# Performance work log

Measured on AMD Instinct MI355X. Metric: run time of the kernel, lower is better.

The kernel has to match this reference:

```python
import jax, jax.numpy as jnp
import numpy as np

GAMMA = -0.1   # l0_gamma
ZETA = 1.1     # l0_zeta
BETA = 0.66    # l0_beta (hard-concrete temperature)
LAMBDA = 0.01  # lambda_reg (post-warmup current_lambda)
EPS = 1e-12


def _layernorm(x, g, b, eps=1e-5):
    mu = jnp.mean(x, axis=-1, keepdims=True)
    var = jnp.var(x, axis=-1, keepdims=True)
    return (x - mu) / jnp.sqrt(var + eps) * g + b


def setup_inputs() -> dict:
    key = jax.random.key(0)
    ks = jax.random.split(key, 12)
    B, N, D, H, E, C = 8, 512, 512, 256, 32, 2
    node_feat = jax.random.normal(ks[0], (B, N, D), jnp.float32)
    labels = jax.random.randint(ks[1], (B,), 0, C)
    a = (jax.random.uniform(ks[2], (B, N, N)) < 0.05).astype(jnp.float32)
    adjs = jnp.maximum(a, jnp.swapaxes(a, 1, 2)) * (1.0 - jnp.eye(N, dtype=jnp.float32))
    masks = jnp.ones((B, N), jnp.float32)
    init = lambda k, shp, fan: jax.random.normal(k, shp, jnp.float32) / np.sqrt(fan).astype(np.float32)
    return {
        "node_feat": node_feat, "labels": labels, "adjs": adjs, "masks": masks,
        # edge scorer MLP: concat([h_i,h_j]) -> edge_dim -> 1, factorized as Wa@h_i + Wb@h_j
        "Wa": init(ks[3], (D, E), D), "Wb": init(ks[4], (D, E), D), "be": jnp.zeros((E,), jnp.float32),
        "W2e": init(ks[5], (E, 1), E), "b2e": jnp.zeros((1,), jnp.float32),
        # conv: Linear(feature_dim, hidden_dim)
        "Wconv": init(ks[6], (D, H), D), "bconv": jnp.zeros((H,), jnp.float32),
        # classifier: Linear(H,H//2) -> ReLU -> LayerNorm -> spectral_norm(Linear(H//2,C))
        "W1c": init(ks[7], (H, H // 2), H), "b1c": jnp.zeros((H // 2,), jnp.float32),
        "ln_g": jnp.ones((H // 2,), jnp.float32), "ln_b": jnp.zeros((H // 2,), jnp.float32),
        "W2c": init(ks[8], (H // 2, C), H // 2), "b2c": jnp.zeros((C,), jnp.float32),
        "u_sn": jax.random.normal(ks[9], (C,), jnp.float32),  # spectral-norm power-iteration buffer
    }


def reference(node_feat, labels, adjs, masks, Wa, Wb, be, W2e, b2e,
              Wconv, bconv, W1c, b1c, ln_g, ln_b, W2c, b2c, u_sn):
    B = node_feat.shape[0]
    # F.normalize(node_feat, p=2, dim=2)
    nrm = jnp.sqrt(jnp.sum(node_feat * node_feat, axis=2, keepdims=True))
    nf = node_feat / jnp.maximum(nrm, EPS)
    # edge scoring: logAlpha[b,i,j] = MLP([h_i ; h_j])
    e1 = nf @ Wa                                  # [B,N,E]
    e2 = nf @ Wb                                  # [B,N,E]
    hpair = jax.nn.relu(e1[:, :, None, :] + e2[:, None, :, :] + be)   # [B,N,N,E]
    logAlpha = jnp.einsum('bije,e->bij', hpair, W2e[:, 0]) + b2e[0]    # [B,N,N]
    # deterministic hard-concrete gate (eval mode): clip(sigmoid(logAlpha)*(zeta-gamma)+gamma, 0, 1)
    gate = jnp.clip(jax.nn.sigmoid(logAlpha) * (ZETA - GAMMA) + GAMMA, 0.0, 1.0)
    edge_weights = gate * adjs
    # aggregate: row-normalized weighted adjacency
    wadj = adjs * edge_weights
    row_sum = jnp.sum(wadj, axis=2, keepdims=True) + 1e-8
    h = jnp.einsum('bij,bjd->bid', wadj / row_sum, nf)
    h = jax.nn.relu(h @ Wconv + bconv)            # [B,N,H]
    # edge-weighted attention pooling: node importance = weighted degree, masked softmax
    imp = jnp.sum(wadj, axis=2)                    # [B,N]
    attn_logits = jnp.where(masks > 0, imp, -1e9)
    attn = jax.nn.softmax(attn_logits, axis=1)
    graph_rep = jnp.einsum('bn,bnh->bh', attn, h)  # [B,H]
    # classifier
    z = jax.nn.relu(graph_rep @ W1c + b1c)
    z = _layernorm(z, ln_g, ln_b)
    # spectral norm (1 power iteration, u/v stop-gradded like torch buffers)
    v = W2c @ u_sn
    v = jax.lax.stop_gradient(v / jnp.maximum(jnp.linalg.norm(v), EPS))
    u2 = W2c.T @ v
    u2 = jax.lax.stop_gradient(u2 / jnp.maximum(jnp.linalg.norm(u2), EPS))
    sigma = v @ (W2c @ u2)
    logits = z @ (W2c / sigma) + b2c              # [B,C]
    # losses
    logp = jax.nn.log_softmax(logits, axis=1)
    cls_loss = -jnp.mean(logp[jnp.arange(B), labels])
    l0_penalty = jnp.sum(jax.nn.sigmoid(logAlpha - BETA * jnp.log(-GAMMA / ZETA)))
    total_loss = cls_loss + LAMBDA * l0_penalty
    return logits, total_loss, adjs * edge_weights
```

## Files before the change

kernel.cpp:

```cpp
#include <hip/hip_runtime.h>


#define Bsz 8
#define Nn  512
#define Dd  512
#define Hh  256
#define Ee  32

#define WS_NFCPK  0L
#define WS_E1     524288L
#define WS_E2     655360L
#define WS_WADJB  786432L
#define WS_RS     1835008L
#define WS_L0     1839104L
#define WS_GR     1839112L
#define WS_WABPK  1841160L
#define WS_WCPK   1857544L

typedef __bf16 bf16x8 __attribute__((ext_vector_type(8)));
typedef float  f32x4  __attribute__((ext_vector_type(4)));

__device__ inline ushort f2bf(float f) {
  union { float f; unsigned u; } c; c.f = f;
  return (ushort)((c.u + 0x7fffu + ((c.u >> 16) & 1u)) >> 16);
}

__global__ __launch_bounds__(256) void pack_weights(
    const float* __restrict__ Wconv, const float* __restrict__ Wa,
    const float* __restrict__ Wb, ushort* __restrict__ wcpk,
    ushort* __restrict__ wabpk)
{
  const int g = blockIdx.x*256 + threadIdx.x;
  if (g < 16384) {
    const int kq = g >> 8, n = g & 255;
    ushort tmp[8];
    #pragma unroll
    for (int j = 0; j < 8; ++j) tmp[j] = f2bf(Wconv[(kq*8 + j)*Hh + n]);
    *(uint4*)(wcpk + (long)g*8) = *(uint4*)tmp;
  } else if (g < 16384 + 4096) {
    const int gg = g - 16384;
    const int kq = gg >> 6, n = gg & 63;
    const float* W = (n < 32) ? Wa : Wb;
    const int e = n & 31;
    ushort tmp[8];
    #pragma unroll
    for (int j = 0; j < 8; ++j) tmp[j] = f2bf(W[(kq*8 + j)*Ee + e]);
    *(uint4*)(wabpk + (long)gg*8) = *(uint4*)tmp;
  }
}

__global__ __launch_bounds__(256) void norm_e12_nfc(
    const float* __restrict__ nfeat, const ushort* __restrict__ wabpk,
    const ushort* __restrict__ wcpk, const float* __restrict__ be,
    ushort* __restrict__ nfcpk, float* __restrict__ e1, float* __restrict__ e2,
    float* __restrict__ row_sum, float* __restrict__ gr,
    float* __restrict__ l0_sum)
{
  const int blk = blockIdx.x;
  const int r0 = blk*16;
  const int b = r0 >> 9;
  const int t = threadIdx.x;
  const int r = t >> 4;
  const int seg = t & 15;

  __shared__ ushort As[(63*17 + 15 + 1)*8];
  __shared__ ushort BsA[2][4*64*8];
  __shared__ ushort BsC[2][4*256*8];

  float4 v[8];
  const float* src = nfeat + (long)(r0 + r)*Dd + seg*32;
  #pragma unroll
  for (int i = 0; i < 8; ++i) v[i] = *(const float4*)(src + i*4);
  float s = 0.f;
  #pragma unroll
  for (int i = 0; i < 8; ++i)
    s += v[i].x*v[i].x + v[i].y*v[i].y + v[i].z*v[i].z + v[i].w*v[i].w;
  #pragma unroll
  for (int m = 1; m < 16; m <<= 1) s += __shfl_xor(s, m, 16);
  const float sc = 1.f / fmaxf(sqrtf(s), 1e-12f);
  #pragma unroll
  for (int q = 0; q < 4; ++q) {
    ushort tmp[8];
    const float4 a = v[2*q], bq = v[2*q+1];
    tmp[0]=f2bf(a.x*sc);  tmp[1]=f2bf(a.y*sc);  tmp[2]=f2bf(a.z*sc);  tmp[3]=f2bf(a.w*sc);
    tmp[4]=f2bf(bq.x*sc); tmp[5]=f2bf(bq.y*sc); tmp[6]=f2bf(bq.z*sc); tmp[7]=f2bf(bq.w*sc);
    *(uint4*)(As + ((seg*4 + q)*17 + r)*8) = *(uint4*)tmp;
  }
  if (t < 16) row_sum[r0 + t] = 0.f;
  if (blk == 0) {
    for (int p = t; p < Bsz*Hh; p += 256) gr[p] = 0.f;
    if (t == 0) *l0_sum = 0.f;
  }

  const int lane = t & 63, l15 = lane & 15, quad = lane >> 4;
  const int w = t >> 6;
  const int abq = t >> 6, abn = t & 63;

  f32x4 acc_e = {0.f, 0.f, 0.f, 0.f};
  f32x4 acc_c[4];
  #pragma unroll
  for (int j = 0; j < 4; ++j) acc_c[j] = (f32x4){0.f,0.f,0.f,0.f};

  uint4 pab = *(const uint4*)(wabpk + ((long)abq*64 + abn)*8);
  uint4 pc[4];
  #pragma unroll
  for (int p = 0; p < 4; ++p) {
    const int g = t + p*256;
    pc[p] = *(const uint4*)(wcpk + ((long)(g >> 8)*256 + (g & 255))*8);
  }
  *(uint4*)(BsA[0] + (abq*64 + abn)*8) = pab;
  #pragma unroll
  for (int p = 0; p < 4; ++p) {
    const int g = t + p*256;
    *(uint4*)(BsC[0] + ((g >> 8)*256 + (g & 255))*8) = pc[p];
  }
  {
    pab = *(const uint4*)(wabpk + ((long)(4 + abq)*64 + abn)*8);
    #pragma unroll
    for (int p = 0; p < 4; ++p) {
      const int g = t + p*256;
      pc[p] = *(const uint4*)(wcpk + ((long)(4 + (g >> 8))*256 + (g & 255))*8);
    }
  }

  for (int k0 = 0; k0 < 512; k0 += 32) {
    const int pb = (k0 >> 5) & 1;
    __syncthreads();
    if (k0 + 32 < 512) {
      *(uint4*)(BsA[1-pb] + (abq*64 + abn)*8) = pab;
      #pragma unroll
      for (int p = 0; p < 4; ++p) {
        const int g = t + p*256;
        *(uint4*)(BsC[1-pb] + ((g >> 8)*256 + (g & 255))*8) = pc[p];
      }
      if (k0 + 64 < 512) {
        const int kb = (k0 + 64) >> 3;
        pab = *(const uint4*)(wabpk + ((long)(kb + abq)*64 + abn)*8);
        #pragma unroll
        for (int p = 0; p < 4; ++p) {
          const int g = t + p*256;
          pc[p] = *(const uint4*)(wcpk + ((long)(kb + (g >> 8))*256 + (g & 255))*8);
        }
      }
    }
    const bf16x8 af = *(const bf16x8*)(As + (((k0 >> 3) + quad)*17 + l15)*8);
    const bf16x8 bfa = *(const bf16x8*)(BsA[pb] + (quad*64 + w*16 + l15)*8);
    acc_e = __builtin_amdgcn_mfma_f32_16x16x32_bf16(af, bfa, acc_e, 0, 0, 0);
    #pragma unroll
    for (int fn = 0; fn < 4; ++fn) {
      const bf16x8 bfc = *(const bf16x8*)(BsC[pb] + (quad*256 + w*64 + fn*16 + l15)*8);
      acc_c[fn] = __builtin_amdgcn_mfma_f32_16x16x32_bf16(af, bfc, acc_c[fn], 0, 0, 0);
    }
  }

  {
    const int col = w*16 + l15;
    #pragma unroll
    for (int rr = 0; rr < 4; ++rr) {
      const int row = r0 + quad*4 + rr;
      if (col < 32) e1[(long)row*Ee + col] = acc_e[rr] + be[col];
      else          e2[(long)row*Ee + (col - 32)] = acc_e[rr];
    }
  }

  __syncthreads();
  ushort* tile = BsC[0];
  #pragma unroll
  for (int fn = 0; fn < 4; ++fn) {
    const int col = w*64 + fn*16 + l15;
    #pragma unroll
    for (int rr = 0; rr < 4; ++rr)
      tile[(quad*4 + rr)*260 + col] = f2bf(acc_c[fn][rr]);
  }
  __syncthreads();
  #pragma unroll
  for (int p = 0; p < 2; ++p) {
    const int g = t + p*256;
    const int oct = g >> 8, c = g & 255;
    ushort tmp[8];
    #pragma unroll
    for (int j = 0; j < 8; ++j) tmp[j] = tile[(oct*8 + j)*260 + c];
    const long og = ((r0 & 511) >> 3) + oct;
    *(uint4*)(nfcpk + ((long)b*16384 + og*256 + c)*8) = *(uint4*)tmp;
  }
}

__global__ __launch_bounds__(256) void edge_kernel(
    const float* __restrict__ e1, const float* __restrict__ e2,
    const float* __restrict__ W2e, const float* __restrict__ b2e,
    const float* __restrict__ adjs, float* __restrict__ out_wadj,
    ushort* __restrict__ wadj_b, float* __restrict__ row_sum,
    float* __restrict__ l0_sum)
{
  const int b  = blockIdx.z;
  const int i0 = blockIdx.y * 32;
  const int j0 = blockIdx.x * 128;
  const int t  = threadIdx.x;

  __shared__ float e2s[32*132];

  #pragma unroll
  for (int itr = 0; itr < 4; ++itr) {
    const int idx = t + itr*256;
    const int kq = idx & 7, jg = idx >> 3;
    const float4 v = *(const float4*)(e2 + ((long)(b*Nn + j0 + jg))*Ee + kq*4);
    e2s[(kq*4+0)*132 + jg] = v.x;
    e2s[(kq*4+1)*132 + jg] = v.y;
    e2s[(kq*4+2)*132 + jg] = v.z;
    e2s[(kq*4+3)*132 + jg] = v.w;
  }

  const int pair  = t >> 4;
  const int jslot = t & 15;
  const int ia = i0 + pair*2;
  const int ib = ia + 1;
  const int ja = jslot*4;
  const int jb = ja + 64;

  float e1af[32], e1bf[32], w2f[32];
  #pragma unroll
  for (int q = 0; q < 8; ++q) {
    *(float4*)(&e1af[q*4]) = *(const float4*)(e1 + ((long)(b*Nn + ia))*Ee + q*4);
    *(float4*)(&e1bf[q*4]) = *(const float4*)(e1 + ((long)(b*Nn + ib))*Ee + q*4);
    *(float4*)(&w2f[q*4])  = *(const float4*)(W2e + q*4);
  }
  const float b2 = b2e[0];
  __syncthreads();

  float acc[2][8] = {};
  #pragma unroll
  for (int k = 0; k < 32; ++k) {
    const float4 va = *(const float4*)(e2s + k*132 + ja);
    const float4 vb = *(const float4*)(e2s + k*132 + jb);
    const float w = w2f[k];
    const float ea = e1af[k], eb = e1bf[k];
    acc[0][0] += fmaxf(ea+va.x, 0.f)*w;
    acc[0][1] += fmaxf(ea+va.y, 0.f)*w;
    acc[0][2] += fmaxf(ea+va.z, 0.f)*w;
    acc[0][3] += fmaxf(ea+va.w, 0.f)*w;
    acc[0][4] += fmaxf(ea+vb.x, 0.f)*w;
    acc[0][5] += fmaxf(ea+vb.y, 0.f)*w;
    acc[0][6] += fmaxf(ea+vb.z, 0.f)*w;
    acc[0][7] += fmaxf(ea+vb.w, 0.f)*w;
    acc[1][0] += fmaxf(eb+va.x, 0.f)*w;
    acc[1][1] += fmaxf(eb+va.y, 0.f)*w;
    acc[1][2] += fmaxf(eb+va.z, 0.f)*w;
    acc[1][3] += fmaxf(eb+va.w, 0.f)*w;
    acc[1][4] += fmaxf(eb+vb.x, 0.f)*w;
    acc[1][5] += fmaxf(eb+vb.y, 0.f)*w;
    acc[1][6] += fmaxf(eb+vb.z, 0.f)*w;
    acc[1][7] += fmaxf(eb+vb.w, 0.f)*w;
  }

  float rs[2] = {0.f, 0.f};
  float l0acc = 0.f;
  #pragma unroll
  for (int ii = 0; ii < 2; ++ii) {
    const int i = (ii == 0) ? ia : ib;
    const float* arow = adjs     + ((long)(b*Nn + i))*Nn + j0;
    ushort* bwrow     = wadj_b   + ((long)(b*Nn + i))*Nn + j0;
    float* outrow     = out_wadj + ((long)(b*Nn + i))*Nn + j0;
    #pragma unroll
    for (int h2 = 0; h2 < 2; ++h2) {
      const int jl = (h2 == 0) ? ja : jb;
      const float4 av = *(const float4*)(arow + jl);
      float wv[4];
      #pragma unroll
      for (int c = 0; c < 4; ++c) {
        const float logA = acc[ii][h2*4 + c] + b2;
        const float sg = 1.f/(1.f + expf(-logA));
        const float gate = fminf(fmaxf(sg*1.2f - 0.1f, 0.f), 1.f);
        const float a = (c==0)?av.x:(c==1)?av.y:(c==2)?av.z:av.w;
        const float w = gate*a*a;
        wv[c] = w;
        rs[ii] += w;
        l0acc += 1.f/(1.f + expf(-(logA + 1.58261088f)));
      }
      ushort4 bw;
      bw.x = f2bf(wv[0]); bw.y = f2bf(wv[1]); bw.z = f2bf(wv[2]); bw.w = f2bf(wv[3]);
      *(ushort4*)(bwrow + jl) = bw;
      outrow[jl+0] = wv[0]; outrow[jl+1] = wv[1];
      outrow[jl+2] = wv[2]; outrow[jl+3] = wv[3];
    }
  }

  #pragma unroll
  for (int m = 1; m < 16; m <<= 1) {
    rs[0] += __shfl_xor(rs[0], m, 16);
    rs[1] += __shfl_xor(rs[1], m, 16);
  }
  if (jslot == 0) {
    atomicAdd(&row_sum[b*Nn + ia], rs[0]);
    atomicAdd(&row_sum[b*Nn + ib], rs[1]);
  }
  #pragma unroll
  for (int m = 1; m < 64; m <<= 1) l0acc += __shfl_xor(l0acc, m, 64);
  if ((t & 63) == 0) atomicAdd(l0_sum, l0acc);
}

__global__ __launch_bounds__(256) void gemm_pool(
    const ushort* __restrict__ wadjb, const ushort* __restrict__ nfcpk,
    const float* __restrict__ row_sum, const float* __restrict__ masks,
    const float* __restrict__ bconv, float* __restrict__ gr)
{
  const int bb = blockIdx.z;
  const int m0 = blockIdx.y*64, n0 = blockIdx.x*64;
  const int t = threadIdx.x;
  const int lane = t & 63, l15 = lane & 15, quad = lane >> 4;
  const int wv = t >> 6, wr = wv & 1, wc = wv >> 1;

  __shared__ ushort As[2][259*8];
  __shared__ ushort Bs[2][256*8];
  __shared__ float ptile[64*65];
  __shared__ float red[256];
  __shared__ float attn_s[64];
  __shared__ float mx_s, sinv_s;

  const ushort* Ab = wadjb + (long)bb*262144;
  const ushort* Bb = nfcpk + (long)bb*131072;
  const int am = t >> 2, akq = t & 3;
  const int bn = t & 63, bkq = t >> 6;

  f32x4 acc[2][2];
  #pragma unroll
  for (int i = 0; i < 2; ++i)
    #pragma unroll
    for (int j = 0; j < 2; ++j) acc[i][j] = (f32x4){0.f,0.f,0.f,0.f};

  uint4 ra = *(const uint4*)(Ab + (long)(m0+am)*512 + akq*8);
  uint4 rb = *(const uint4*)(Bb + ((long)bkq*256 + n0 + bn)*8);
  *(uint4*)(As[0] + (akq*65 + am)*8) = ra;
  *(uint4*)(Bs[0] + (bkq*64 + bn)*8) = rb;
  ra = *(const uint4*)(Ab + (long)(m0+am)*512 + 32 + akq*8);
  rb = *(const uint4*)(Bb + ((long)(4 + bkq)*256 + n0 + bn)*8);

  for (int k0 = 0; k0 < 512; k0 += 32) {
    const int pb = (k0 >> 5) & 1;
    __syncthreads();
    if (k0 + 32 < 512) {
      *(uint4*)(As[1-pb] + (akq*65 + am)*8) = ra;
      *(uint4*)(Bs[1-pb] + (bkq*64 + bn)*8) = rb;
      if (k0 + 64 < 512) {
        ra = *(const uint4*)(Ab + (long)(m0+am)*512 + (k0+64) + akq*8);
        rb = *(const uint4*)(Bb + ((long)(((k0+64) >> 3) + bkq)*256 + n0 + bn)*8);
      }
    }
    bf16x8 af[2], bfr[2];
    #pragma unroll
    for (int i = 0; i < 2; ++i)
      af[i] = *(const bf16x8*)(As[pb] + (quad*65 + wr*32 + i*16 + l15)*8);
    #pragma unroll
    for (int j = 0; j < 2; ++j)
      bfr[j] = *(const bf16x8*)(Bs[pb] + (quad*64 + wc*32 + j*16 + l15)*8);
    #pragma unroll
    for (int i = 0; i < 2; ++i)
      #pragma unroll
      for (int j = 0; j < 2; ++j)
        acc[i][j] = __builtin_amdgcn_mfma_f32_16x16x32_bf16(
            af[i], bfr[j], acc[i][j], 0, 0, 0);
  }
  __syncthreads();

  {
    const float mk0 = masks[bb*Nn + t], mk1 = masks[bb*Nn + t + 256];
    const float lv0 = (mk0 > 0.f) ? row_sum[bb*Nn + t] : -1e9f;
    const float lv1 = (mk1 > 0.f) ? row_sum[bb*Nn + t + 256] : -1e9f;
    red[t] = fmaxf(lv0, lv1); __syncthreads();
    for (int s = 128; s > 0; s >>= 1) { if (t < s) red[t] = fmaxf(red[t], red[t+s]); __syncthreads(); }
    if (t == 0) mx_s = red[0];
    __syncthreads();
    const float mx = mx_s;
    red[t] = expf(lv0 - mx) + expf(lv1 - mx); __syncthreads();
    for (int s = 128; s > 0; s >>= 1) { if (t < s) red[t] += red[t+s]; __syncthreads(); }
    if (t == 0) sinv_s = 1.f/red[0];
    __syncthreads();
    if (t < 64) {
      const int node = m0 + t;
      const float mm = masks[bb*Nn + node];
      const float lv = (mm > 0.f) ? row_sum[bb*Nn + node] : -1e9f;
      attn_s[t] = expf(lv - mx)*sinv_s;
    }
    __syncthreads();
  }

  #pragma unroll
  for (int i = 0; i < 2; ++i) {
    #pragma unroll
    for (int j = 0; j < 2; ++j) {
      const int lcol = wc*32 + j*16 + l15;
      const float bias = bconv[n0 + lcol];
      #pragma unroll
      for (int rr = 0; rr < 4; ++rr) {
        const int lrow = wr*32 + i*16 + quad*4 + rr;
        const int row = m0 + lrow;
        const float scl = 1.f/(row_sum[bb*Nn + row] + 1e-8f);
        const float hv = fmaxf(acc[i][j][rr]*scl + bias, 0.f);
        ptile[lrow*65 + lcol] = hv * attn_s[lrow];
      }
    }
  }
  __syncthreads();
  if (t < 64) {
    float s = 0.f;
    #pragma unroll 4
    for (int rr = 0; rr < 64; ++rr) s += ptile[rr*65 + t];
    atomicAdd(&gr[bb*Hh + n0 + t], s);
  }
}

__global__ __launch_bounds__(256) void classifier_kernel(
    const float* __restrict__ gr, const float* __restrict__ W1c,
    const float* __restrict__ b1c, const float* __restrict__ ln_g,
    const float* __restrict__ ln_b, const float* __restrict__ W2c,
    const float* __restrict__ b2c, const float* __restrict__ u_sn,
    const int* __restrict__ labels, const float* __restrict__ l0_sum,
    float* __restrict__ out)
{
  const int t = threadIdx.x;
  __shared__ float grs[2048];
  __shared__ float z[8][128];
  __shared__ float red[256];
  __shared__ float vv[128];
  __shared__ float mu_s[8], ri_s[8];
  __shared__ float lg[16];
  for (int p = t; p < 2048; p += 256) grs[p] = gr[p];
  __syncthreads();
  #pragma unroll
  for (int p = 0; p < 4; ++p) {
    const int idx = t + p*256;
    const int b = idx >> 7, o = idx & 127;
    float acc = b1c[o];
    for (int d = 0; d < 256; ++d) acc += grs[b*256 + d]*W1c[d*128 + o];
    z[b][o] = fmaxf(acc, 0.f);
  }
  __syncthreads();
  if (t < 8) {
    float mu = 0.f;
    for (int o = 0; o < 128; ++o) mu += z[t][o];
    mu *= (1.f/128.f);
    float var = 0.f;
    for (int o = 0; o < 128; ++o) { const float d = z[t][o]-mu; var += d*d; }
    var *= (1.f/128.f);
    mu_s[t] = mu; ri_s[t] = rsqrtf(var + 1e-5f);
  }
  const float u0 = u_sn[0], u1 = u_sn[1];
  float vt = 0.f;
  if (t < 128) { vt = W2c[2*t]*u0 + W2c[2*t+1]*u1; vv[t] = vt; }
  red[t] = (t < 128) ? vt*vt : 0.f;
  __syncthreads();
  for (int s = 128; s > 0; s >>= 1) { if (t < s) red[t] += red[t+s]; __syncthreads(); }
  const float vninv = 1.f/fmaxf(sqrtf(red[0]), 1e-12f);
  __syncthreads();
  red[t] = (t < 128) ? W2c[2*t]*vv[t]*vninv : 0.f;
  __syncthreads();
  for (int s = 128; s > 0; s >>= 1) { if (t < s) red[t] += red[t+s]; __syncthreads(); }
  const float u20 = red[0];
  __syncthreads();
  red[t] = (t < 128) ? W2c[2*t+1]*vv[t]*vninv : 0.f;
  __syncthreads();
  for (int s = 128; s > 0; s >>= 1) { if (t < s) red[t] += red[t+s]; __syncthreads(); }
  const float u21 = red[0];
  __syncthreads();
  const float uninv = 1.f/fmaxf(sqrtf(u20*u20 + u21*u21), 1e-12f);
  const float u2n0 = u20*uninv, u2n1 = u21*uninv;
  red[t] = (t < 128) ? vv[t]*vninv*(W2c[2*t]*u2n0 + W2c[2*t+1]*u2n1) : 0.f;
  __syncthreads();
  for (int s = 128; s > 0; s >>= 1) { if (t < s) red[t] += red[t+s]; __syncthreads(); }
  const float sinv = 1.f/red[0];
  __syncthreads();
  if (t < 16) {
    const int b = t >> 1, c = t & 1;
    const float mu = mu_s[b], ri = ri_s[b];
    float acc = 0.f;
    for (int o = 0; o < 128; ++o) {
      const float zln = (z[b][o]-mu)*ri*ln_g[o] + ln_b[o];
      acc += zln*W2c[2*o + c];
    }
    const float lgv = acc*sinv + b2c[c];
    lg[t] = lgv;
    out[t] = lgv;
  }
  __syncthreads();
  if (t == 0) {
    float closs = 0.f;
    for (int b = 0; b < 8; ++b) {
      const float a0 = lg[2*b], a1 = lg[2*b+1];
      const float m = fmaxf(a0, a1);
      const float lse = m + logf(expf(a0-m) + expf(a1-m));
      closs += lse - lg[2*b + labels[b]];
    }
    closs *= (1.f/8.f);
    out[16] = closs + 0.01f*l0_sum[0];
  }
}

extern "C" void kernel_launch(void* const* d_in, const int* in_sizes, int n_in,
                              void* d_out, int out_size, void* d_ws, size_t ws_size,
                              hipStream_t stream) {
  const float* node_feat = (const float*)d_in[0];
  const int*   labels    = (const int*)d_in[1];
  const float* adjs      = (const float*)d_in[2];
  const float* masks     = (const float*)d_in[3];
  const float* Wa        = (const float*)d_in[4];
  const float* Wb        = (const float*)d_in[5];
  const float* be        = (const float*)d_in[6];
  const float* W2e       = (const float*)d_in[7];
  const float* b2e       = (const float*)d_in[8];
  const float* Wconv     = (const float*)d_in[9];
  const float* bconv     = (const float*)d_in[10];
  const float* W1c       = (const float*)d_in[11];
  const float* b1c       = (const float*)d_in[12];
  const float* ln_g      = (const float*)d_in[13];
  const float* ln_b      = (const float*)d_in[14];
  const float* W2c       = (const float*)d_in[15];
  const float* b2c       = (const float*)d_in[16];
  const float* u_sn      = (const float*)d_in[17];

  float* out = (float*)d_out;
  float* ws  = (float*)d_ws;
  ushort* nfcpk  = (ushort*)(ws + WS_NFCPK);
  float*  e1     = ws + WS_E1;
  float*  e2     = ws + WS_E2;
  ushort* wadjb  = (ushort*)(ws + WS_WADJB);
  float*  row_sum= ws + WS_RS;
  float*  l0s    = ws + WS_L0;
  float*  gr     = ws + WS_GR;
  ushort* wabpk  = (ushort*)(ws + WS_WABPK);
  ushort* wcpk   = (ushort*)(ws + WS_WCPK);

  pack_weights<<<80, 256, 0, stream>>>(Wconv, Wa, Wb, wcpk, wabpk);
  norm_e12_nfc<<<256, 256, 0, stream>>>(node_feat, wabpk, wcpk, be, nfcpk,
                                        e1, e2, row_sum, gr, l0s);
  edge_kernel<<<dim3(Nn/128, Nn/32, Bsz), 256, 0, stream>>>(
      e1, e2, W2e, b2e, adjs, out + 17, wadjb, row_sum, l0s);
  gemm_pool<<<dim3(Hh/64, Nn/64, Bsz), 256, 0, stream>>>(
      wadjb, nfcpk, row_sum, masks, bconv, gr);
  classifier_kernel<<<1, 256, 0, stream>>>(gr, W1c, b1c, ln_g, ln_b, W2c, b2c,
                                           u_sn, labels, l0s, out);
}
```

Baseline: 195.3 us.

## Replace shared-memory tree reductions with wave shuffles and reuse sigmoid exponential

The edge kernel now reuses the single exp(-logA) for the L0 penalty sigmoid, using exp(-(x+c)) = exp(-x)*exp(-c), which halves transcendental calls per edge. The pooling kernel's softmax max and sum reductions and the classifier kernel's layernorm, spectral-norm and logit reductions switch from barrier-heavy shared-memory trees to wavefront shuffle reductions with a few shared partials. The change targets instruction count and the long chains of __syncthreads in these small kernels. Numerics change slightly because summation order differs and the exp factoring introduces small rounding differences.

Result: slower. 212.7 us (+8.9%).

```diff
diff --git a/kernel.cpp b/kernel.cpp
--- a/kernel.cpp
+++ b/kernel.cpp
@@ -268,13 +268,14 @@
       #pragma unroll
       for (int c = 0; c < 4; ++c) {
         const float logA = acc[ii][h2*4 + c] + b2;
-        const float sg = 1.f/(1.f + expf(-logA));
+        const float e = expf(-logA);
+        const float sg = 1.f/(1.f + e);
         const float gate = fminf(fmaxf(sg*1.2f - 0.1f, 0.f), 1.f);
         const float a = (c==0)?av.x:(c==1)?av.y:(c==2)?av.z:av.w;
         const float w = gate*a*a;
         wv[c] = w;
         rs[ii] += w;
-        l0acc += 1.f/(1.f + expf(-(logA + 1.58261088f)));
+        l0acc += 1.f/(1.f + 0.20543832f*e);
       }
       ushort4 bw;
       bw.x = f2bf(wv[0]); bw.y = f2bf(wv[1]); bw.z = f2bf(wv[2]); bw.w = f2bf(wv[3]);
@@ -312,9 +313,8 @@
   __shared__ ushort As[2][259*8];
   __shared__ ushort Bs[2][256*8];
   __shared__ float ptile[64*65];
-  __shared__ float red[256];
+  __shared__ float red[8];
   __shared__ float attn_s[64];
-  __shared__ float mx_s, sinv_s;
 
   const ushort* Ab = wadjb + (long)bb*262144;
   const ushort* Bb = nfcpk + (long)bb*131072;
@@ -365,20 +365,23 @@
     const float mk0 = masks[bb*Nn + t], mk1 = masks[bb*Nn + t + 256];
     const float lv0 = (mk0 > 0.f) ? row_sum[bb*Nn + t] : -1e9f;
     const float lv1 = (mk1 > 0.f) ? row_sum[bb*Nn + t + 256] : -1e9f;
-    red[t] = fmaxf(lv0, lv1); __syncthreads();
-    for (int s = 128; s > 0; s >>= 1) { if (t < s) red[t] = fmaxf(red[t], red[t+s]); __syncthreads(); }
-    if (t == 0) mx_s = red[0];
+    float m = fmaxf(lv0, lv1);
+    #pragma unroll
+    for (int s = 1; s < 64; s <<= 1) m = fmaxf(m, __shfl_xor(m, s, 64));
+    if (lane == 0) red[wv] = m;
     __syncthreads();
-    const float mx = mx_s;
-    red[t] = expf(lv0 - mx) + expf(lv1 - mx); __syncthreads();
-    for (int s = 128; s > 0; s >>= 1) { if (t < s) red[t] += red[t+s]; __syncthreads(); }
-    if (t == 0) sinv_s = 1.f/red[0];
+    const float mx = fmaxf(fmaxf(red[0], red[1]), fmaxf(red[2], red[3]));
+    float sm = expf(lv0 - mx) + expf(lv1 - mx);
+    #pragma unroll
+    for (int s = 1; s < 64; s <<= 1) sm += __shfl_xor(sm, s, 64);
+    if (lane == 0) red[4 + wv] = sm;
     __syncthreads();
+    const float sinv = 1.f/(red[4] + red[5] + red[6] + red[7]);
     if (t < 64) {
       const int node = m0 + t;
       const float mm = masks[bb*Nn + node];
       const float lv = (mm > 0.f) ? row_sum[bb*Nn + node] : -1e9f;
-      attn_s[t] = expf(lv - mx)*sinv_s;
+      attn_s[t] = expf(lv - mx)*sinv;
     }
     __syncthreads();
   }
@@ -419,78 +422,99 @@
   const int t = threadIdx.x;
   __shared__ float grs[2048];
   __shared__ float z[8][128];
-  __shared__ float red[256];
-  __shared__ float vv[128];
   __shared__ float mu_s[8], ri_s[8];
+  __shared__ float part[6];
+  __shared__ float sinv_s;
   __shared__ float lg[16];
+
   for (int p = t; p < 2048; p += 256) grs[p] = gr[p];
   __syncthreads();
+
   #pragma unroll
   for (int p = 0; p < 4; ++p) {
     const int idx = t + p*256;
     const int b = idx >> 7, o = idx & 127;
     float acc = b1c[o];
+    #pragma unroll 4
     for (int d = 0; d < 256; ++d) acc += grs[b*256 + d]*W1c[d*128 + o];
     z[b][o] = fmaxf(acc, 0.f);
   }
   __syncthreads();
-  if (t < 8) {
-    float mu = 0.f;
-    for (int o = 0; o < 128; ++o) mu += z[t][o];
-    mu *= (1.f/128.f);
-    float var = 0.f;
-    for (int o = 0; o < 128; ++o) { const float d = z[t][o]-mu; var += d*d; }
-    var *= (1.f/128.f);
-    mu_s[t] = mu; ri_s[t] = rsqrtf(var + 1e-5f);
-  }
-  const float u0 = u_sn[0], u1 = u_sn[1];
-  float vt = 0.f;
-  if (t < 128) { vt = W2c[2*t]*u0 + W2c[2*t+1]*u1; vv[t] = vt; }
-  red[t] = (t < 128) ? vt*vt : 0.f;
-  __syncthreads();
-  for (int s = 128; s > 0; s >>= 1) { if (t < s) red[t] += red[t+s]; __syncthreads(); }
-  const float vninv = 1.f/fmaxf(sqrtf(red[0]), 1e-12f);
-  __syncthreads();
-  red[t] = (t < 128) ? W2c[2*t]*vv[t]*vninv : 0.f;
-  __syncthreads();
-  for (int s = 128; s > 0; s >>= 1) { if (t < s) red[t] += red[t+s]; __syncthreads(); }
-  const float u20 = red[0];
-  __syncthreads();
-  red[t] = (t < 128) ? W2c[2*t+1]*vv[t]*vninv : 0.f;
-  __syncthreads();
-  for (int s = 128; s > 0; s >>= 1) { if (t < s) red[t] += red[t+s]; __syncthreads(); }
-  const float u21 = red[0];
-  __syncthreads();
-  const float uninv = 1.f/fmaxf(sqrtf(u20*u20 + u21*u21), 1e-12f);
-  const float u2n0 = u20*uninv, u2n1 = u21*uninv;
-  red[t] = (t < 128) ? vv[t]*vninv*(W2c[2*t]*u2n0 + W2c[2*t+1]*u2n1) : 0.f;
-  __syncthreads();
-  for (int s = 128; s > 0; s >>= 1) { if (t < s) red[t] += red[t+s]; __syncthreads(); }
-  const float sinv = 1.f/red[0];
-  __syncthreads();
-  if (t < 16) {
-    const int b = t >> 1, c = t & 1;
+
+  {
+    const int b = t >> 5, g = t & 31;
+    const float4 zv = *(const float4*)(&z[b][g*4]);
+    float s1 = zv.x + zv.y + zv.z + zv.w;
+    #pragma unroll
+    for (int m = 1; m < 32; m <<= 1) s1 += __shfl_xor(s1, m, 32);
+    const float mu = s1*(1.f/128.f);
+    float s2 = (zv.x-mu)*(zv.x-mu) + (zv.y-mu)*(zv.y-mu)
+             + (zv.z-mu)*(zv.z-mu) + (zv.w-mu)*(zv.w-mu);
+    #pragma unroll
+    for (int m = 1; m < 32; m <<= 1) s2 += __shfl_xor(s2, m, 32);
+    if (g == 0) { mu_s[b] = mu; ri_s[b] = rsqrtf(s2*(1.f/128.f) + 1e-5f); }
+  }
+
+  if (t < 128) {
+    const float w0 = W2c[2*t], w1 = W2c[2*t+1];
+    const float vt = w0*u_sn[0] + w1*u_sn[1];
+    float svv = vt*vt, sa = vt*w0, sb = vt*w1;
+    #pragma unroll
+    for (int m = 1; m < 64; m <<= 1) {
+      svv += __shfl_xor(svv, m, 64);
+      sa  += __shfl_xor(sa , m, 64);
+      sb  += __shfl_xor(sb , m, 64);
+    }
+    if ((t & 63) == 0) {
+      const int w = t >> 6;
+      part[w*3+0] = svv; part[w*3+1] = sa; part[w*3+2] = sb;
+    }
+  }
+  __syncthreads();
+  if (t == 0) {
+    const float svv = part[0] + part[3];
+    const float sa  = part[1] + part[4];
+    const float sb  = part[2] + part[5];
+    const float vninv = 1.f/fmaxf(sqrtf(svv), 1e-12f);
+    const float u20 = sa*vninv, u21 = sb*vninv;
+    const float uninv = 1.f/fmaxf(sqrtf(u20*u20 + u21*u21), 1e-12f);
+    const float u2n0 = u20*uninv, u2n1 = u21*uninv;
+    const float sigma = vninv*(u2n0*sa + u2n1*sb);
+    sinv_s = 1.f/sigma;
+  }
+  __syncthreads();
+
+  {
+    const float sinv = sinv_s;
+    const int grp = t >> 4, g = t & 15;
+    const int b = grp >> 1, c = grp & 1;
     const float mu = mu_s[b], ri = ri_s[b];
     float acc = 0.f;
-    for (int o = 0; o < 128; ++o) {
+    #pragma unroll
+    for (int j = 0; j < 8; ++j) {
+      const int o = g*8 + j;
       const float zln = (z[b][o]-mu)*ri*ln_g[o] + ln_b[o];
       acc += zln*W2c[2*o + c];
     }
-    const float lgv = acc*sinv + b2c[c];
-    lg[t] = lgv;
-    out[t] = lgv;
+    #pragma unroll
+    for (int m = 1; m < 16; m <<= 1) acc += __shfl_xor(acc, m, 16);
+    if (g == 0) {
+      const float lgv = acc*sinv + b2c[c];
+      lg[grp] = lgv;
+      out[grp] = lgv;
+    }
   }
   __syncthreads();
   if (t == 0) {
     float closs = 0.f;
+    #pragma unroll
     for (int b = 0; b < 8; ++b) {
       const float a0 = lg[2*b], a1 = lg[2*b+1];
       const float m = fmaxf(a0, a1);
       const float lse = m + logf(expf(a0-m) + expf(a1-m));
       closs += lse - lg[2*b + labels[b]];
     }
-    closs *= (1.f/8.f);
-    out[16] = closs + 0.01f*l0_sum[0];
+    out[16] = closs*(1.f/8.f) + 0.01f*l0_sum[0];
   }
 }
 
```
